# Kernel optimization log

Hardware: AMD Instinct MI355X
Metric: run time of the kernel (lower is better)

## Reference

```python
import jax, jax.numpy as jnp
import numpy as np

BASE = 7.0
TWO_PI = 2.0 * np.pi
MAX_PATHS = 9

def _mod_phase(x):
    # ModularPhaseNorm(hidden, base=7): periodic phase nonlinearity
    return jnp.sin(TWO_PI * x / BASE)

def _branch(data, W):
    # data: [N, F, P], W: [O, F] -> [N, O, 3P] with per-path (neg, zero, pos) branches
    pos = jnp.einsum('nfp,of->nop', data, W)
    n, o, p = pos.shape
    tri = jnp.stack([-pos, jnp.zeros_like(pos), pos], axis=-1)  # [N,O,P,3]
    return tri.reshape(n, o, p * 3)

def _scorer(data, w1, b1, w2, b2):
    # data: [N, F, P] -> scores [N, P]  (linear -> modular phase -> linear)
    z = _mod_phase(jnp.einsum('nfp,hf->nph', data, w1) + b1)
    return (jnp.einsum('nph,oh->npo', z, w2) + b2)[..., 0]

def _prune(data, weights):
    # keep top-k paths by softmax weight, renormalize kept weights
    w_k, idx = jax.lax.top_k(weights, MAX_PATHS)
    data_k = jnp.take_along_axis(data, idx[:, None, :], axis=2)
    w_k = w_k / jnp.clip(jnp.sum(w_k, axis=1, keepdims=True), 1e-8)
    return data_k, w_k

def _forward(x, W1, W2, Wout, s1a_w, s1a_b, s1b_w, s1b_b, s2a_w, s2a_b, s2b_w, s2b_b, soa_w, soa_b, sob_w, sob_b):
    batch, choices, dims = x.shape
    data = x.reshape(batch * choices, dims)[:, :, None]  # 1 path
    weights = None
    for W, aw, ab, bw, bb in ((W1, s1a_w, s1a_b, s1b_w, s1b_b),
                              (W2, s2a_w, s2a_b, s2b_w, s2b_b)):
        data = jnp.tanh(_branch(data, W))
        weights = jax.nn.softmax(_scorer(data, aw, ab, bw, bb), axis=1)
        if data.shape[2] > MAX_PATHS:  # static shape condition
            data, weights = _prune(data, weights)
    data = _branch(data, Wout)  # [N, 1, 27]
    weights = jax.nn.softmax(_scorer(data, soa_w, soa_b, sob_w, sob_b), axis=1)
    if data.shape[2] > MAX_PATHS:
        data, weights = _prune(data, weights)
    out = jnp.sum(data * weights[:, None, :], axis=2)  # weighted collapse -> [N, 1]
    return out.reshape(batch, choices)

def setup_inputs():
    key = jax.random.key(0)
    ks = jax.random.split(key, 12)
    B, C, D, H, SH, SHO = 64, 64, 1024, 1024, 64, 32
    def lin(k, o, i):
        return jax.random.normal(k, (o, i), jnp.float32) / np.sqrt(i)
    return {
        'x': jax.random.normal(ks[0], (B, C, D), jnp.float32),
        'W1': lin(ks[1], H, D),
        'W2': lin(ks[2], H, H),
        'Wout': lin(ks[3], 1, H),
        's1a_w': lin(ks[4], SH, H), 's1a_b': jnp.zeros((SH,), jnp.float32),
        's1b_w': lin(ks[5], 1, SH), 's1b_b': jnp.zeros((1,), jnp.float32),
        's2a_w': lin(ks[6], SH, H), 's2a_b': jnp.zeros((SH,), jnp.float32),
        's2b_w': lin(ks[7], 1, SH), 's2b_b': jnp.zeros((1,), jnp.float32),
        'soa_w': lin(ks[8], SHO, 1), 'soa_b': jnp.zeros((SHO,), jnp.float32),
        'sob_w': lin(ks[9], 1, SHO), 'sob_b': jnp.zeros((1,), jnp.float32),
    }

def reference(x, W1, W2, Wout, s1a_w, s1a_b, s1b_w, s1b_b, s2a_w, s2a_b, s2b_w, s2b_b, soa_w, soa_b, sob_w, sob_b):
    return _forward(x, W1, W2, Wout, s1a_w, s1a_b, s1b_w, s1b_b, s2a_w, s2a_b, s2b_w, s2b_b, soa_w, soa_b, sob_w, sob_b)
```

## Files before the change

### kernel.cpp

```cpp
#include <hip/hip_runtime.h>


typedef __attribute__((ext_vector_type(4))) float     f32x4;
typedef __attribute__((ext_vector_type(8))) _Float16  f16x8;

#define AS1 __attribute__((address_space(1)))
#define AS3 __attribute__((address_space(3)))
#define GLOAD16(gp, lp) \
    __builtin_amdgcn_global_load_lds((AS1 const void*)(gp), (AS3 void*)(lp), 16, 0, 0)

__global__ __launch_bounds__(256)
void pbcs_cvt(const float* __restrict__ x,  _Float16* __restrict__ xo,
              const float* __restrict__ w1, _Float16* __restrict__ w1o,
              const float* __restrict__ w2, _Float16* __restrict__ w2o)
{
    const int b = blockIdx.x;
    const float* src; _Float16* dst; int idx;
    if (b < 2048)      { src = x;  dst = xo;  idx = b * 256 + threadIdx.x; }
    else if (b < 2560) { src = w1; dst = w1o; idx = (b - 2048) * 256 + threadIdx.x; }
    else               { src = w2; dst = w2o; idx = (b - 2560) * 256 + threadIdx.x; }
    const float4 v0 = ((const float4*)src)[idx * 2];
    const float4 v1 = ((const float4*)src)[idx * 2 + 1];
    f16x8 h;
    h[0] = (_Float16)v0.x; h[1] = (_Float16)v0.y;
    h[2] = (_Float16)v0.z; h[3] = (_Float16)v0.w;
    h[4] = (_Float16)v1.x; h[5] = (_Float16)v1.y;
    h[6] = (_Float16)v1.z; h[7] = (_Float16)v1.w;
    ((f16x8*)dst)[idx] = h;
}

template<int EPI>
__global__ __launch_bounds__(256, 2)
void pbcs_gemm16(const _Float16* __restrict__ A, const _Float16* __restrict__ B,
                 _Float16* __restrict__ Cout, const float* __restrict__ wout,
                 float* __restrict__ s_part)
{
    __shared__ char smem[2][32768];

    const int tid  = threadIdx.x;
    const int lane = tid & 63;
    const int wid  = tid >> 6;
    const int wm   = wid >> 1;
    const int wn   = wid & 1;
    const int l15  = lane & 15;
    const int g    = lane >> 4;

    const int b  = blockIdx.x;
    const int bm = (b & 7) * 4 + ((b >> 3) & 3);
    const int bn = b >> 5;

    const char* aS[4]; const char* bS[4]; int aD[4], bD[4];
#pragma unroll
    for (int j = 0; j < 4; ++j) {
        const int c = wid * 4 + j;
        const int r = c * 8 + (lane >> 3), s = lane & 7;
        aS[j] = (const char*)A + (size_t)(bm * 128 + r) * 2048 + 16 * (s ^ (r & 7));
        aD[j] = c * 1024;
        bS[j] = (const char*)B + (size_t)(bn * 128 + r) * 2048 + 16 * (s ^ (r & 7));
        bD[j] = 16384 + c * 1024;
    }

    int aoff[4][2], boff[4][2];
#pragma unroll
    for (int f = 0; f < 4; ++f) {
        const int ra = wm * 64 + f * 16 + l15;
        const int rb = wn * 64 + f * 16 + l15;
#pragma unroll
        for (int kh = 0; kh < 2; ++kh) {
            aoff[f][kh] = ra * 128 + 16 * (((kh << 2) | g) ^ (ra & 7));
            boff[f][kh] = 16384 + rb * 128 + 16 * (((kh << 2) | g) ^ (rb & 7));
        }
    }

    f32x4 acc[4][4];
#pragma unroll
    for (int i = 0; i < 4; ++i)
#pragma unroll
        for (int j = 0; j < 4; ++j) acc[i][j] = (f32x4)0.f;

#define STAGE(buf, kt) do {                                      \
        const int _ko = (kt) * 128;                              \
        _Pragma("unroll")                                        \
        for (int _j = 0; _j < 4; ++_j) {                         \
            GLOAD16(aS[_j] + _ko, smem[buf] + aD[_j]);           \
            GLOAD16(bS[_j] + _ko, smem[buf] + bD[_j]);           \
        }                                                        \
    } while (0)

#define COMPUTE(buf) do {                                                        \
        _Pragma("unroll")                                                        \
        for (int _kh = 0; _kh < 2; ++_kh) {                                      \
            f16x8 _a[4], _b[4];                                                  \
            _Pragma("unroll")                                                    \
            for (int _f = 0; _f < 4; ++_f) {                                     \
                _a[_f] = *(const f16x8*)(smem[buf] + aoff[_f][_kh]);             \
                _b[_f] = *(const f16x8*)(smem[buf] + boff[_f][_kh]);             \
            }                                                                    \
            _Pragma("unroll")                                                    \
            for (int _mf = 0; _mf < 4; ++_mf)                                    \
            _Pragma("unroll")                                                    \
            for (int _nf = 0; _nf < 4; ++_nf)                                    \
                acc[_mf][_nf] = __builtin_amdgcn_mfma_f32_16x16x32_f16(          \
                    _a[_mf], _b[_nf], acc[_mf][_nf], 0, 0, 0);                   \
        }                                                                        \
    } while (0)

    STAGE(0, 0);
    STAGE(1, 1);
#pragma unroll 1
    for (int t = 0; t < 15; ++t) {
        asm volatile("s_waitcnt vmcnt(8)" ::: "memory");
        __builtin_amdgcn_s_barrier();
        __builtin_amdgcn_sched_barrier(0);
        COMPUTE(t & 1);
        asm volatile("s_waitcnt lgkmcnt(0)" ::: "memory");
        __builtin_amdgcn_sched_barrier(0);
        __builtin_amdgcn_s_barrier();
        if (t < 14) STAGE(t & 1, t + 2);
    }
    asm volatile("s_waitcnt vmcnt(0)" ::: "memory");
    __builtin_amdgcn_s_barrier();
    __builtin_amdgcn_sched_barrier(0);
    COMPUTE(1);

    if (EPI == 0) {
#pragma unroll
        for (int mf = 0; mf < 4; ++mf)
#pragma unroll
        for (int nf = 0; nf < 4; ++nf)
#pragma unroll
        for (int jj = 0; jj < 4; ++jj) {
            const int row = bm * 128 + wm * 64 + mf * 16 + g * 4 + jj;
            const int col = bn * 128 + wn * 64 + nf * 16 + l15;
            Cout[(size_t)row * 1024 + col] = (_Float16)tanhf(acc[mf][nf][jj]);
        }
    } else {
        float w[4];
#pragma unroll
        for (int nf = 0; nf < 4; ++nf)
            w[nf] = wout[bn * 128 + wn * 64 + nf * 16 + l15];
#pragma unroll
        for (int mf = 0; mf < 4; ++mf)
#pragma unroll
        for (int jj = 0; jj < 4; ++jj) {
            float v = 0.f;
#pragma unroll
            for (int nf = 0; nf < 4; ++nf)
                v += tanhf(acc[mf][nf][jj]) * w[nf];
            v += __shfl_xor(v, 1, 64);
            v += __shfl_xor(v, 2, 64);
            v += __shfl_xor(v, 4, 64);
            v += __shfl_xor(v, 8, 64);
            if (l15 == 0) {
                const int row = bm * 128 + wm * 64 + mf * 16 + g * 4 + jj;
                s_part[row * 16 + bn * 2 + wn] = v;
            }
        }
    }
#undef STAGE
#undef COMPUTE
}

__global__ __launch_bounds__(256)
void pbcs_finalize(const float* __restrict__ s_part,
                   const float* __restrict__ soa_w, const float* __restrict__ soa_b,
                   const float* __restrict__ sob_w, const float* __restrict__ sob_b,
                   float* __restrict__ out, int Nrows)
{
    const int row  = blockIdx.x * 4 + (threadIdx.x >> 6);
    const int lane = threadIdx.x & 63;
    if (row >= Nrows) return;

    float part = (lane < 16) ? s_part[row * 16 + lane] : 0.f;
#pragma unroll
    for (int off = 32; off > 0; off >>= 1) part += __shfl_xor(part, off, 64);
    const float s = part;

    const float C7 = 0.8975979010256552f;
    float tS = 0.f, tZ = 0.f, tN = 0.f;
    if (lane < 32) {
        const float aw = soa_w[lane];
        const float ab = soa_b[lane];
        const float bw = sob_w[lane];
        tS = bw * sinf(C7 * fmaf(aw,  s, ab));
        tZ = bw * sinf(C7 * ab);
        tN = bw * sinf(C7 * fmaf(aw, -s, ab));
    }
#pragma unroll
    for (int off = 32; off > 0; off >>= 1) {
        tS += __shfl_xor(tS, off, 64);
        tZ += __shfl_xor(tZ, off, 64);
        tN += __shfl_xor(tN, off, 64);
    }
    const float bb = sob_b[0];
    const float fS = tS + bb;
    const float f0 = tZ + bb;
    const float fN = tN + bb;

    const int j  = lane;
    const int kk = j / 3;
    const int q  = j - kk * 3;
    const int p  = ((0x101 >> kk) & 1) - ((0x044 >> kk) & 1);
    const int c  = (q == 0) ? -p : ((q == 2) ? p : 0);
    const float val = (float)c * s;
    const float sc  = (c == 0) ? f0 : ((c > 0) ? fS : fN);

    int rank = 0;
#pragma unroll 1
    for (int i = 0; i < 27; ++i) {
        const float sci = __shfl(sc, i, 64);
        rank += (sci > sc) || (sci == sc && i < j);
    }
    const float mx = fmaxf(fS, fmaxf(f0, fN));
    float e = (j < 27 && rank < 9) ? expf(sc - mx) : 0.f;
    float num = val * e;
    float den = e;
#pragma unroll
    for (int off = 32; off > 0; off >>= 1) {
        num += __shfl_xor(num, off, 64);
        den += __shfl_xor(den, off, 64);
    }
    if (lane == 0) out[row] = num / den;
}

extern "C" void kernel_launch(void* const* d_in, const int* in_sizes, int n_in,
                              void* d_out, int out_size, void* d_ws, size_t ws_size,
                              hipStream_t stream)
{
    const float* x     = (const float*)d_in[0];
    const float* W1    = (const float*)d_in[1];
    const float* W2    = (const float*)d_in[2];
    const float* Wout  = (const float*)d_in[3];
    const float* soa_w = (const float*)d_in[12];
    const float* soa_b = (const float*)d_in[13];
    const float* sob_w = (const float*)d_in[14];
    const float* sob_b = (const float*)d_in[15];

    const int Nr = 4096;
    char* ws = (char*)d_ws;
    _Float16* xf  = (_Float16*)ws;
    _Float16* t1f = (_Float16*)(ws + (8u  << 20));
    _Float16* w1f = (_Float16*)(ws + (16u << 20));
    _Float16* w2f = (_Float16*)(ws + (18u << 20));
    float* s_part = (float*)(ws + (20u << 20));

    pbcs_cvt<<<3072, 256, 0, stream>>>(x, xf, W1, w1f, W2, w2f);

    pbcs_gemm16<0><<<256, 256, 0, stream>>>(xf,  w1f, t1f, nullptr, nullptr);
    pbcs_gemm16<1><<<256, 256, 0, stream>>>(t1f, w2f, nullptr, Wout, s_part);

    pbcs_finalize<<<Nr / 4, 256, 0, stream>>>(s_part, soa_w, soa_b, sob_w, sob_b,
                                              (float*)d_out, Nr);
}
```

Measured before the change: 56.30 us.

## Fuse convert, two GEMMs and finalize into one cooperative kernel with grid syncs

Replaces four separate launches (fp32→fp16 conversion, two GEMMs, finalize) with a single cooperative kernel of 256 blocks that runs the phases in sequence, separated by grid.sync(). The conversion and finalize phases become grid-stride loops over the same 256 blocks. The aim is to remove per-launch overhead and the gaps between kernels. In exchange, the convert and finalize phases run on far fewer blocks than before, and each grid-wide barrier adds its own cost.

```diff
diff --git a/kernel.cpp b/kernel.cpp
--- a/kernel.cpp
+++ b/kernel.cpp
@@ -1,4 +1,7 @@
 #include <hip/hip_runtime.h>
+#include <hip/hip_cooperative_groups.h>
+
+namespace cg = cooperative_groups;
 
 
 typedef __attribute__((ext_vector_type(4))) float     f32x4;
@@ -9,34 +12,12 @@
 #define GLOAD16(gp, lp) \
     __builtin_amdgcn_global_load_lds((AS1 const void*)(gp), (AS3 void*)(lp), 16, 0, 0)
 
-__global__ __launch_bounds__(256)
-void pbcs_cvt(const float* __restrict__ x,  _Float16* __restrict__ xo,
-              const float* __restrict__ w1, _Float16* __restrict__ w1o,
-              const float* __restrict__ w2, _Float16* __restrict__ w2o)
+template<int EPI>
+__device__ __forceinline__
+void gemm_phase(char* sm, const _Float16* __restrict__ A,
+                const _Float16* __restrict__ B, _Float16* __restrict__ Cout,
+                const float* __restrict__ wout, float* __restrict__ s_part)
 {
-    const int b = blockIdx.x;
-    const float* src; _Float16* dst; int idx;
-    if (b < 2048)      { src = x;  dst = xo;  idx = b * 256 + threadIdx.x; }
-    else if (b < 2560) { src = w1; dst = w1o; idx = (b - 2048) * 256 + threadIdx.x; }
-    else               { src = w2; dst = w2o; idx = (b - 2560) * 256 + threadIdx.x; }
-    const float4 v0 = ((const float4*)src)[idx * 2];
-    const float4 v1 = ((const float4*)src)[idx * 2 + 1];
-    f16x8 h;
-    h[0] = (_Float16)v0.x; h[1] = (_Float16)v0.y;
-    h[2] = (_Float16)v0.z; h[3] = (_Float16)v0.w;
-    h[4] = (_Float16)v1.x; h[5] = (_Float16)v1.y;
-    h[6] = (_Float16)v1.z; h[7] = (_Float16)v1.w;
-    ((f16x8*)dst)[idx] = h;
-}
-
-template<int EPI>
-__global__ __launch_bounds__(256, 2)
-void pbcs_gemm16(const _Float16* __restrict__ A, const _Float16* __restrict__ B,
-                 _Float16* __restrict__ Cout, const float* __restrict__ wout,
-                 float* __restrict__ s_part)
-{
-    __shared__ char smem[2][32768];
-
     const int tid  = threadIdx.x;
     const int lane = tid & 63;
     const int wid  = tid >> 6;
@@ -80,21 +61,23 @@
 
 #define STAGE(buf, kt) do {                                      \
         const int _ko = (kt) * 128;                              \
+        char* _D = sm + (buf) * 32768;                           \
         _Pragma("unroll")                                        \
         for (int _j = 0; _j < 4; ++_j) {                         \
-            GLOAD16(aS[_j] + _ko, smem[buf] + aD[_j]);           \
-            GLOAD16(bS[_j] + _ko, smem[buf] + bD[_j]);           \
+            GLOAD16(aS[_j] + _ko, _D + aD[_j]);                  \
+            GLOAD16(bS[_j] + _ko, _D + bD[_j]);                  \
         }                                                        \
     } while (0)
 
 #define COMPUTE(buf) do {                                                        \
+        const char* _L = sm + (buf) * 32768;                                     \
         _Pragma("unroll")                                                        \
         for (int _kh = 0; _kh < 2; ++_kh) {                                      \
             f16x8 _a[4], _b[4];                                                  \
             _Pragma("unroll")                                                    \
             for (int _f = 0; _f < 4; ++_f) {                                     \
-                _a[_f] = *(const f16x8*)(smem[buf] + aoff[_f][_kh]);             \
-                _b[_f] = *(const f16x8*)(smem[buf] + boff[_f][_kh]);             \
+                _a[_f] = *(const f16x8*)(_L + aoff[_f][_kh]);                    \
+                _b[_f] = *(const f16x8*)(_L + boff[_f][_kh]);                    \
             }                                                                    \
             _Pragma("unroll")                                                    \
             for (int _mf = 0; _mf < 4; ++_mf)                                    \
@@ -161,66 +144,100 @@
 #undef COMPUTE
 }
 
-__global__ __launch_bounds__(256)
-void pbcs_finalize(const float* __restrict__ s_part,
-                   const float* __restrict__ soa_w, const float* __restrict__ soa_b,
-                   const float* __restrict__ sob_w, const float* __restrict__ sob_b,
-                   float* __restrict__ out, int Nrows)
+__global__ __launch_bounds__(256, 2)
+void pbcs_fused(const float* __restrict__ x,  _Float16* __restrict__ xf,
+                const float* __restrict__ w1, _Float16* __restrict__ w1f,
+                const float* __restrict__ w2, _Float16* __restrict__ w2f,
+                const float* __restrict__ wout, _Float16* __restrict__ t1f,
+                float* __restrict__ s_part,
+                const float* __restrict__ soa_w, const float* __restrict__ soa_b,
+                const float* __restrict__ sob_w, const float* __restrict__ sob_b,
+                float* __restrict__ out)
 {
-    const int row  = blockIdx.x * 4 + (threadIdx.x >> 6);
+    __shared__ char smem[2][32768];
+    cg::grid_group grid = cg::this_grid();
+
+#pragma unroll 1
+    for (int it = 0; it < 12; ++it) {
+        const int vb = blockIdx.x + it * 256;
+        const float* src; _Float16* dst; int idx;
+        if (vb < 2048)      { src = x;  dst = xf;  idx = vb * 256 + threadIdx.x; }
+        else if (vb < 2560) { src = w1; dst = w1f; idx = (vb - 2048) * 256 + threadIdx.x; }
+        else                { src = w2; dst = w2f; idx = (vb - 2560) * 256 + threadIdx.x; }
+        const float4 v0 = ((const float4*)src)[idx * 2];
+        const float4 v1 = ((const float4*)src)[idx * 2 + 1];
+        f16x8 h;
+        h[0] = (_Float16)v0.x; h[1] = (_Float16)v0.y;
+        h[2] = (_Float16)v0.z; h[3] = (_Float16)v0.w;
+        h[4] = (_Float16)v1.x; h[5] = (_Float16)v1.y;
+        h[6] = (_Float16)v1.z; h[7] = (_Float16)v1.w;
+        ((f16x8*)dst)[idx] = h;
+    }
+    grid.sync();
+
+    gemm_phase<0>(&smem[0][0], xf, w1f, t1f, nullptr, nullptr);
+    grid.sync();
+
+    gemm_phase<1>(&smem[0][0], t1f, w2f, nullptr, wout, s_part);
+    grid.sync();
+
     const int lane = threadIdx.x & 63;
-    if (row >= Nrows) return;
-
-    float part = (lane < 16) ? s_part[row * 16 + lane] : 0.f;
-#pragma unroll
-    for (int off = 32; off > 0; off >>= 1) part += __shfl_xor(part, off, 64);
-    const float s = part;
-
-    const float C7 = 0.8975979010256552f;
-    float tS = 0.f, tZ = 0.f, tN = 0.f;
-    if (lane < 32) {
-        const float aw = soa_w[lane];
-        const float ab = soa_b[lane];
-        const float bw = sob_w[lane];
-        tS = bw * sinf(C7 * fmaf(aw,  s, ab));
-        tZ = bw * sinf(C7 * ab);
-        tN = bw * sinf(C7 * fmaf(aw, -s, ab));
-    }
-#pragma unroll
-    for (int off = 32; off > 0; off >>= 1) {
-        tS += __shfl_xor(tS, off, 64);
-        tZ += __shfl_xor(tZ, off, 64);
-        tN += __shfl_xor(tN, off, 64);
-    }
-    const float bb = sob_b[0];
-    const float fS = tS + bb;
-    const float f0 = tZ + bb;
-    const float fN = tN + bb;
-
-    const int j  = lane;
-    const int kk = j / 3;
-    const int q  = j - kk * 3;
-    const int p  = ((0x101 >> kk) & 1) - ((0x044 >> kk) & 1);
-    const int c  = (q == 0) ? -p : ((q == 2) ? p : 0);
-    const float val = (float)c * s;
-    const float sc  = (c == 0) ? f0 : ((c > 0) ? fS : fN);
-
-    int rank = 0;
-#pragma unroll 1
-    for (int i = 0; i < 27; ++i) {
-        const float sci = __shfl(sc, i, 64);
-        rank += (sci > sc) || (sci == sc && i < j);
-    }
-    const float mx = fmaxf(fS, fmaxf(f0, fN));
-    float e = (j < 27 && rank < 9) ? expf(sc - mx) : 0.f;
-    float num = val * e;
-    float den = e;
-#pragma unroll
-    for (int off = 32; off > 0; off >>= 1) {
-        num += __shfl_xor(num, off, 64);
-        den += __shfl_xor(den, off, 64);
-    }
-    if (lane == 0) out[row] = num / den;
+    const int gw   = blockIdx.x * 4 + (threadIdx.x >> 6);
+#pragma unroll 1
+    for (int rr = 0; rr < 4; ++rr) {
+        const int row = gw * 4 + rr;
+
+        float part = (lane < 16) ? s_part[row * 16 + lane] : 0.f;
+#pragma unroll
+        for (int off = 32; off > 0; off >>= 1) part += __shfl_xor(part, off, 64);
+        const float s = part;
+
+        const float C7 = 0.8975979010256552f;
+        float tS = 0.f, tZ = 0.f, tN = 0.f;
+        if (lane < 32) {
+            const float aw = soa_w[lane];
+            const float ab = soa_b[lane];
+            const float bw = sob_w[lane];
+            tS = bw * sinf(C7 * fmaf(aw,  s, ab));
+            tZ = bw * sinf(C7 * ab);
+            tN = bw * sinf(C7 * fmaf(aw, -s, ab));
+        }
+#pragma unroll
+        for (int off = 32; off > 0; off >>= 1) {
+            tS += __shfl_xor(tS, off, 64);
+            tZ += __shfl_xor(tZ, off, 64);
+            tN += __shfl_xor(tN, off, 64);
+        }
+        const float bb = sob_b[0];
+        const float fS = tS + bb;
+        const float f0 = tZ + bb;
+        const float fN = tN + bb;
+
+        const int j  = lane;
+        const int kk = j / 3;
+        const int q  = j - kk * 3;
+        const int p  = ((0x101 >> kk) & 1) - ((0x044 >> kk) & 1);
+        const int c  = (q == 0) ? -p : ((q == 2) ? p : 0);
+        const float val = (float)c * s;
+        const float sc  = (c == 0) ? f0 : ((c > 0) ? fS : fN);
+
+        int rank = 0;
+#pragma unroll 1
+        for (int i = 0; i < 27; ++i) {
+            const float sci = __shfl(sc, i, 64);
+            rank += (sci > sc) || (sci == sc && i < j);
+        }
+        const float mx = fmaxf(fS, fmaxf(f0, fN));
+        float e = (j < 27 && rank < 9) ? expf(sc - mx) : 0.f;
+        float num = val * e;
+        float den = e;
+#pragma unroll
+        for (int off = 32; off > 0; off >>= 1) {
+            num += __shfl_xor(num, off, 64);
+            den += __shfl_xor(den, off, 64);
+        }
+        if (lane == 0) out[row] = num / den;
+    }
 }
 
 extern "C" void kernel_launch(void* const* d_in, const int* in_sizes, int n_in,
@@ -236,19 +253,21 @@
     const float* sob_w = (const float*)d_in[14];
     const float* sob_b = (const float*)d_in[15];
 
-    const int Nr = 4096;
     char* ws = (char*)d_ws;
     _Float16* xf  = (_Float16*)ws;
     _Float16* t1f = (_Float16*)(ws + (8u  << 20));
     _Float16* w1f = (_Float16*)(ws + (16u << 20));
     _Float16* w2f = (_Float16*)(ws + (18u << 20));
     float* s_part = (float*)(ws + (20u << 20));
-
-    pbcs_cvt<<<3072, 256, 0, stream>>>(x, xf, W1, w1f, W2, w2f);
-
-    pbcs_gemm16<0><<<256, 256, 0, stream>>>(xf,  w1f, t1f, nullptr, nullptr);
-    pbcs_gemm16<1><<<256, 256, 0, stream>>>(t1f, w2f, nullptr, Wout, s_part);
-
-    pbcs_finalize<<<Nr / 4, 256, 0, stream>>>(s_part, soa_w, soa_b, sob_w, sob_b,
-                                              (float*)d_out, Nr);
+    float* outp   = (float*)d_out;
+
+    void* args[] = {
+        (void*)&x,  (void*)&xf,  (void*)&W1, (void*)&w1f,
+        (void*)&W2, (void*)&w2f, (void*)&Wout, (void*)&t1f,
+        (void*)&s_part,
+        (void*)&soa_w, (void*)&soa_b, (void*)&sob_w, (void*)&sob_b,
+        (void*)&outp
+    };
+    hipLaunchCooperativeKernel((const void*)pbcs_fused, dim3(256), dim3(256),
+                               args, 0, stream);
 }
```

New measurement: 150.7 us. +167.7%, slower.

## Fuse finalize into second GEMM epilogue via last-block atomic counter

Applied to the files above, without the earlier changes.

Removes the separate finalize kernel launch by having the last of the 8 column blocks for each row tile, found with an atomic counter, compute the scorer, top-k and weighted collapse for its 128 rows. The counter is zeroed inside the conversion kernel. This drops one launch and the launch gap, but puts a serial per-thread loop (32 sinf, 27-step rank) on the tail of the last-finishing blocks, and adds threadfence/atomic synchronization.

```diff
diff --git a/kernel.cpp b/kernel.cpp
--- a/kernel.cpp
+++ b/kernel.cpp
@@ -12,9 +12,11 @@
 __global__ __launch_bounds__(256)
 void pbcs_cvt(const float* __restrict__ x,  _Float16* __restrict__ xo,
               const float* __restrict__ w1, _Float16* __restrict__ w1o,
-              const float* __restrict__ w2, _Float16* __restrict__ w2o)
+              const float* __restrict__ w2, _Float16* __restrict__ w2o,
+              int* __restrict__ cnt)
 {
     const int b = blockIdx.x;
+    if (b == 0 && threadIdx.x < 32) cnt[threadIdx.x] = 0;
     const float* src; _Float16* dst; int idx;
     if (b < 2048)      { src = x;  dst = xo;  idx = b * 256 + threadIdx.x; }
     else if (b < 2560) { src = w1; dst = w1o; idx = (b - 2048) * 256 + threadIdx.x; }
@@ -33,7 +35,10 @@
 __global__ __launch_bounds__(256, 2)
 void pbcs_gemm16(const _Float16* __restrict__ A, const _Float16* __restrict__ B,
                  _Float16* __restrict__ Cout, const float* __restrict__ wout,
-                 float* __restrict__ s_part)
+                 float* __restrict__ s_part, int* __restrict__ cnt,
+                 const float* __restrict__ soa_w, const float* __restrict__ soa_b,
+                 const float* __restrict__ sob_w, const float* __restrict__ sob_b,
+                 float* __restrict__ out)
 {
     __shared__ char smem[2][32768];
 
@@ -156,71 +161,68 @@
                 s_part[row * 16 + bn * 2 + wn] = v;
             }
         }
+
+        __shared__ int lastFlag;
+        __syncthreads();
+        if (tid == 0) {
+            __threadfence();
+            lastFlag = (atomicAdd(&cnt[bm], 1) == 7);
+        }
+        __syncthreads();
+        if (lastFlag && tid < 128) {
+            __threadfence();
+            const int row = bm * 128 + tid;
+
+            float s = 0.f;
+#pragma unroll
+            for (int i = 0; i < 16; ++i) s += s_part[row * 16 + i];
+
+            const float C7 = 0.8975979010256552f;
+            float tS = 0.f, tZ = 0.f, tN = 0.f;
+#pragma unroll 1
+            for (int h = 0; h < 32; ++h) {
+                const float aw = soa_w[h];
+                const float ab = soa_b[h];
+                const float bw = sob_w[h];
+                tS += bw * sinf(C7 * fmaf(aw,  s, ab));
+                tZ += bw * sinf(C7 * ab);
+                tN += bw * sinf(C7 * fmaf(aw, -s, ab));
+            }
+            const float bb = sob_b[0];
+            const float fS = tS + bb;
+            const float f0 = tZ + bb;
+            const float fN = tN + bb;
+
+            const unsigned mP = (1u<<2) | (1u<<6) | (1u<<18) | (1u<<26);
+            const unsigned mM = (1u<<0) | (1u<<8) | (1u<<20) | (1u<<24);
+            const unsigned mZ = ~(mP | mM) & 0x07FFFFFFu;
+            const float mx = fmaxf(fS, fmaxf(f0, fN));
+            const float eS = expf(fS - mx);
+            const float e0 = expf(f0 - mx);
+            const float eN = expf(fN - mx);
+            float num = 0.f, den = 0.f;
+#pragma unroll 1
+            for (int j = 0; j < 27; ++j) {
+                const int isP = (mP >> j) & 1;
+                const int isM = (mM >> j) & 1;
+                const float scj = isP ? fS : (isM ? fN : f0);
+                const unsigned below = (1u << j) - 1u;
+                int rank = 0;
+                rank += (fS > scj) ? 4  : ((fS == scj) ? __popc(mP & below) : 0);
+                rank += (fN > scj) ? 4  : ((fN == scj) ? __popc(mM & below) : 0);
+                rank += (f0 > scj) ? 19 : ((f0 == scj) ? __popc(mZ & below) : 0);
+                if (rank < 9) {
+                    const float e   = isP ? eS : (isM ? eN : e0);
+                    const float val = isP ? s  : (isM ? -s : 0.f);
+                    num += val * e;
+                    den += e;
+                }
+            }
+            out[row] = num / den;
+        }
     }
 #undef STAGE
 #undef COMPUTE
-}
-
-__global__ __launch_bounds__(256)
-void pbcs_finalize(const float* __restrict__ s_part,
-                   const float* __restrict__ soa_w, const float* __restrict__ soa_b,
-                   const float* __restrict__ sob_w, const float* __restrict__ sob_b,
-                   float* __restrict__ out, int Nrows)
-{
-    const int row  = blockIdx.x * 4 + (threadIdx.x >> 6);
-    const int lane = threadIdx.x & 63;
-    if (row >= Nrows) return;
-
-    float part = (lane < 16) ? s_part[row * 16 + lane] : 0.f;
-#pragma unroll
-    for (int off = 32; off > 0; off >>= 1) part += __shfl_xor(part, off, 64);
-    const float s = part;
-
-    const float C7 = 0.8975979010256552f;
-    float tS = 0.f, tZ = 0.f, tN = 0.f;
-    if (lane < 32) {
-        const float aw = soa_w[lane];
-        const float ab = soa_b[lane];
-        const float bw = sob_w[lane];
-        tS = bw * sinf(C7 * fmaf(aw,  s, ab));
-        tZ = bw * sinf(C7 * ab);
-        tN = bw * sinf(C7 * fmaf(aw, -s, ab));
-    }
-#pragma unroll
-    for (int off = 32; off > 0; off >>= 1) {
-        tS += __shfl_xor(tS, off, 64);
-        tZ += __shfl_xor(tZ, off, 64);
-        tN += __shfl_xor(tN, off, 64);
-    }
-    const float bb = sob_b[0];
-    const float fS = tS + bb;
-    const float f0 = tZ + bb;
-    const float fN = tN + bb;
-
-    const int j  = lane;
-    const int kk = j / 3;
-    const int q  = j - kk * 3;
-    const int p  = ((0x101 >> kk) & 1) - ((0x044 >> kk) & 1);
-    const int c  = (q == 0) ? -p : ((q == 2) ? p : 0);
-    const float val = (float)c * s;
-    const float sc  = (c == 0) ? f0 : ((c > 0) ? fS : fN);
-
-    int rank = 0;
-#pragma unroll 1
-    for (int i = 0; i < 27; ++i) {
-        const float sci = __shfl(sc, i, 64);
-        rank += (sci > sc) || (sci == sc && i < j);
-    }
-    const float mx = fmaxf(fS, fmaxf(f0, fN));
-    float e = (j < 27 && rank < 9) ? expf(sc - mx) : 0.f;
-    float num = val * e;
-    float den = e;
-#pragma unroll
-    for (int off = 32; off > 0; off >>= 1) {
-        num += __shfl_xor(num, off, 64);
-        den += __shfl_xor(den, off, 64);
-    }
-    if (lane == 0) out[row] = num / den;
 }
 
 extern "C" void kernel_launch(void* const* d_in, const int* in_sizes, int n_in,
@@ -236,19 +238,20 @@
     const float* sob_w = (const float*)d_in[14];
     const float* sob_b = (const float*)d_in[15];
 
-    const int Nr = 4096;
     char* ws = (char*)d_ws;
     _Float16* xf  = (_Float16*)ws;
     _Float16* t1f = (_Float16*)(ws + (8u  << 20));
     _Float16* w1f = (_Float16*)(ws + (16u << 20));
     _Float16* w2f = (_Float16*)(ws + (18u << 20));
     float* s_part = (float*)(ws + (20u << 20));
-
-    pbcs_cvt<<<3072, 256, 0, stream>>>(x, xf, W1, w1f, W2, w2f);
-
-    pbcs_gemm16<0><<<256, 256, 0, stream>>>(xf,  w1f, t1f, nullptr, nullptr);
-    pbcs_gemm16<1><<<256, 256, 0, stream>>>(t1f, w2f, nullptr, Wout, s_part);
-
-    pbcs_finalize<<<Nr / 4, 256, 0, stream>>>(s_part, soa_w, soa_b, sob_w, sob_b,
-                                              (float*)d_out, Nr);
+    int*   cnt    = (int*)(ws + (21u << 20));
+
+    pbcs_cvt<<<3072, 256, 0, stream>>>(x, xf, W1, w1f, W2, w2f, cnt);
+
+    pbcs_gemm16<0><<<256, 256, 0, stream>>>(xf,  w1f, t1f, nullptr, nullptr,
+                                            nullptr, nullptr, nullptr,
+                                            nullptr, nullptr, nullptr);
+    pbcs_gemm16<1><<<256, 256, 0, stream>>>(t1f, w2f, nullptr, Wout, s_part,
+                                            cnt, soa_w, soa_b, sob_w, sob_b,
+                                            (float*)d_out);
 }
```

Measured after the change: 79.18 us. 1.41x slower.
